# Performance work log

Hardware: AMD Instinct MI355X
Metric: run time of the kernel (lower is better)

Reference implementation:

```python
import jax, jax.numpy as jnp
import numpy as np

N_FEATURES = 256
HIDDEN = 16
BATCH = 32768


def setup_inputs() -> dict:
    key = jax.random.key(0)
    ks = jax.random.split(key, 8)
    F, H = N_FEATURES, HIDDEN
    x = jax.random.normal(ks[0], (BATCH, F), dtype=jnp.float32)
    # Stacked per-feature subnet params (torch Linear: y = x @ W.T + b)
    s1 = 1.0  # fan_in=1 for fc1
    W1 = jax.random.uniform(ks[1], (F, H), minval=-s1, maxval=s1, dtype=jnp.float32)
    b1 = jax.random.uniform(ks[2], (F, H), minval=-s1, maxval=s1, dtype=jnp.float32)
    s2 = 1.0 / np.sqrt(H)
    W2 = jax.random.uniform(ks[3], (F, H, H), minval=-s2, maxval=s2, dtype=jnp.float32)  # [F, out, in]
    b2 = jax.random.uniform(ks[4], (F, H), minval=-s2, maxval=s2, dtype=jnp.float32)
    W3 = jax.random.uniform(ks[5], (F, H), minval=-s2, maxval=s2, dtype=jnp.float32)  # out=1
    b3 = jax.random.uniform(ks[6], (F,), minval=-s2, maxval=s2, dtype=jnp.float32)
    linear_a = jnp.zeros((F,), dtype=jnp.float32)
    bias_b = jnp.zeros((1,), dtype=jnp.float32)
    return {"x": x, "linear_a": linear_a, "bias_b": bias_b,
            "W1": W1, "b1": b1, "W2": W2, "b2": b2, "W3": W3, "b3": b3}


def reference(x, linear_a, bias_b, W1, b1, W2, b2, W3, b3):
    # lin term: (x * a).sum(1)
    lin = x @ linear_a  # [B]
    # all subnets batched: h1 [B, F, H]
    h1 = jax.nn.relu(x[:, :, None] * W1[None, :, :] + b1[None, :, :])
    # fc2: y = h1 @ W2.T per feature; W2 is [F, out, in]
    h2 = jax.nn.relu(jnp.einsum('bfh,fkh->bfk', h1, W2) + b2[None, :, :])
    # fc3 -> scalar per feature, then sum over features
    out_f = jnp.einsum('bfh,fh->bf', h2, W3) + b3[None, :]  # [B, F]
    add_sum = out_f.sum(axis=1)  # [B]
    logits = lin + bias_b[0] + add_sum
    return logits
```

## Files before the change

### kernel.cpp

```cpp
#include <hip/hip_runtime.h>


typedef float    f32x4 __attribute__((ext_vector_type(4)));
typedef _Float16 f16x4 __attribute__((ext_vector_type(4)));
typedef __fp16   pk16x2 __attribute__((ext_vector_type(2)));

__device__ __forceinline__ f16x4 cvt4(f32x4 v) {
    pk16x2 lo = __builtin_amdgcn_cvt_pkrtz(v[0], v[1]);
    pk16x2 hi = __builtin_amdgcn_cvt_pkrtz(v[2], v[3]);
    union { unsigned u[2]; f16x4 h; } un;
    un.u[0] = __builtin_bit_cast(unsigned, lo);
    un.u[1] = __builtin_bit_cast(unsigned, hi);
    return un.h;
}

__device__ __forceinline__ f16x4 relu_h(f16x4 v) {
    f16x4 z = {};
    return __builtin_elementwise_max(v, z);
}

__device__ __forceinline__ f32x4 relu_f(f32x4 v) {
    f32x4 z = {0.f, 0.f, 0.f, 0.f};
    return __builtin_elementwise_max(v, z);
}

#define FCHUNK 16
#define BATCH  32768

__global__ __launch_bounds__(256, 8) void igann_kernel(
    const float* __restrict__ x,  const float* __restrict__ la,
    const float* __restrict__ bb, const float* __restrict__ W1,
    const float* __restrict__ b1, const float* __restrict__ W2,
    const float* __restrict__ b2, const float* __restrict__ W3,
    const float* __restrict__ b3, float* __restrict__ ws)
{
    const int tid = threadIdx.x;
    const int l   = tid & 63;
    const int w   = tid >> 6;
    const int r   = l & 15;
    const int g   = l >> 4;
    const int g4  = g * 4;

    const int bid = blockIdx.x;
    const int rb  = (bid & 7) + (((bid >> 3) & 15) << 3);
    const int fg  = bid >> 7;
    const int f0  = fg * FCHUNK;
    const int rowbase = rb * 256;

    __shared__ _Float16 xs [256 * 16];
    __shared__ _Float16 w2s[FCHUNK * 16 * 16];
    __shared__ float    wbs_sums[256];
    __shared__ float2   bws[FCHUNK * 16];
    _Float16* wbs = (_Float16*)wbs_sums;
    float*    sums = wbs_sums;

    {
        const int rr  = tid >> 2;
        const int c4g = tid & 3;
        const int sw  = (rr >> 2) & 3;
        #pragma unroll
        for (int it = 0; it < 4; ++it) {
            const int row = it * 64 + rr;
            f32x4 v = *(const f32x4*)(x + (size_t)(rowbase + row) * 256 + f0 + c4g * 4);
            *(f16x4*)(xs + row * 16 + ((c4g ^ sw) & 3) * 4) = cvt4(v);
        }
    }
    {
        const int f = tid >> 4, n = tid & 15;
        const int sw = (n >> 2) & 3;
        const float* src = W2 + ((size_t)(f0 + f) * 16 + n) * 16;
        _Float16* dst = w2s + (f * 16 + n) * 16;
        #pragma unroll
        for (int q = 0; q < 4; ++q) {
            f32x4 v = *(const f32x4*)(src + q * 4);
            *(f16x4*)(dst + ((q ^ sw) & 3) * 4) = cvt4(v);
        }
    }
    {
        const int f = tid >> 4, k = tid & 15;
        const int base = f * 32 + (k >> 2) * 8 + (k & 3);
        wbs[base]     = (_Float16)W1[(size_t)(f0 + f) * 16 + k];
        wbs[base + 4] = (_Float16)b1[(size_t)(f0 + f) * 16 + k];
    }
    {
        const int f = tid >> 4, n = tid & 15;
        bws[tid] = make_float2(b2[(size_t)(f0 + f) * 16 + n],
                               W3[(size_t)(f0 + f) * 16 + n]);
    }
    __syncthreads();

    const _Float16* xw  = xs + (w * 64 + r) * 16;
    const int       xsw = ((w * 64 + r) >> 2) & 3;
    const _Float16* w2p = w2s + r * 16 + ((g ^ ((r >> 2) & 3)) & 3) * 4;

    f32x4 acc[4];
    #pragma unroll
    for (int t = 0; t < 4; ++t) acc[t] = (f32x4){0.f, 0.f, 0.f, 0.f};

    for (int fi = 0; fi < FCHUNK; fi += 4) {
        const int xoff = (((fi >> 2) ^ xsw) & 3) * 4;
        f16x4 xv[4];
        #pragma unroll
        for (int t = 0; t < 4; ++t)
            xv[t] = *(const f16x4*)(xw + t * 256 + xoff);

        #pragma unroll
        for (int u = 0; u < 4; ++u) {
            const int f = fi + u;
            f16x4 w1h   = *(const f16x4*)(wbs + f * 32 + g * 8);
            f16x4 b1h   = *(const f16x4*)(wbs + f * 32 + g * 8 + 4);
            f16x4 bfrag = *(const f16x4*)(w2p + f * 256);
            const float2 bw = bws[f * 16 + r];
            const f32x4 cinit = {bw.x, bw.x, bw.x, bw.x};
            const f32x4 w3k4  = {bw.y, bw.y, bw.y, bw.y};

            #pragma unroll
            for (int t = 0; t < 4; ++t) {
                const _Float16 s = xv[t][u];
                f16x4 xb = {s, s, s, s};
                f16x4 h = relu_h(xb * w1h + b1h);
                f32x4 d = __builtin_amdgcn_mfma_f32_16x16x16f16(h, bfrag, cinit, 0, 0, 0);
                acc[t] = __builtin_elementwise_fma(relu_f(d), w3k4, acc[t]);
            }
        }
    }

    __syncthreads();

    #pragma unroll
    for (int t = 0; t < 4; ++t)
        #pragma unroll
        for (int j = 0; j < 4; ++j) {
            float v = acc[t][j];
            v += __shfl_xor(v, 1, 64);
            v += __shfl_xor(v, 2, 64);
            v += __shfl_xor(v, 4, 64);
            v += __shfl_xor(v, 8, 64);
            if (r == 0)
                sums[w * 64 + t * 16 + g4 + j] = v;
        }
    __syncthreads();

    float b3s = 0.f;
    #pragma unroll
    for (int c = 0; c < FCHUNK; ++c) b3s += b3[f0 + c];
    float lin = 0.f;
    {
        const int swe = (tid >> 2) & 3;
        #pragma unroll
        for (int gq = 0; gq < 4; ++gq) {
            f16x4 xv4 = *(const f16x4*)(xs + tid * 16 + ((gq ^ swe) & 3) * 4);
            #pragma unroll
            for (int e = 0; e < 4; ++e)
                lin = fmaf((float)xv4[e], la[f0 + gq * 4 + e], lin);
        }
    }
    ws[(size_t)fg * BATCH + rowbase + tid] = sums[tid] + lin + b3s;
}

__global__ __launch_bounds__(128) void igann_reduce(
    const float* __restrict__ ws, const float* __restrict__ bb,
    float* __restrict__ out)
{
    const int i = blockIdx.x * 128 + threadIdx.x;
    float s = bb[0];
    #pragma unroll
    for (int gq = 0; gq < 16; ++gq)
        s += ws[(size_t)gq * BATCH + i];
    out[i] = s;
}

extern "C" void kernel_launch(void* const* d_in, const int* in_sizes, int n_in,
                              void* d_out, int out_size, void* d_ws, size_t ws_size,
                              hipStream_t stream) {
    const float* x  = (const float*)d_in[0];
    const float* la = (const float*)d_in[1];
    const float* bb = (const float*)d_in[2];
    const float* W1 = (const float*)d_in[3];
    const float* b1 = (const float*)d_in[4];
    const float* W2 = (const float*)d_in[5];
    const float* b2 = (const float*)d_in[6];
    const float* W3 = (const float*)d_in[7];
    const float* b3 = (const float*)d_in[8];
    float* out = (float*)d_out;
    float* ws  = (float*)d_ws;

    dim3 grid(2048), block(256);
    hipLaunchKernelGGL(igann_kernel, grid, block, 0, stream,
                       x, la, bb, W1, b1, W2, b2, W3, b3, ws);
    hipLaunchKernelGGL(igann_reduce, dim3(256), dim3(128), 0, stream,
                       ws, bb, out);
}
```

Before: 105.8 us.

## Load x directly into registers with software prefetch, drop shared-memory x staging

Drops the shared-memory staging buffer for x. Each thread now loads its own x rows from global memory into registers, converting to fp16 one 4-feature group at a time while prefetching the next group. The linear term is accumulated in registers during the main loop and passed through a small shared array. This removes LDS writes and reads and the swizzle logic, but each lane's global loads are 16-byte strided accesses, 1 KB apart per row, which may coalesce worse and leave latency exposed. Four lanes per row also load the same x data redundantly.

```diff
diff --git a/kernel.cpp b/kernel.cpp
--- a/kernel.cpp
+++ b/kernel.cpp
@@ -47,24 +47,19 @@
     const int f0  = fg * FCHUNK;
     const int rowbase = rb * 256;
 
-    __shared__ _Float16 xs [256 * 16];
     __shared__ _Float16 w2s[FCHUNK * 16 * 16];
     __shared__ float    wbs_sums[256];
     __shared__ float2   bws[FCHUNK * 16];
-    _Float16* wbs = (_Float16*)wbs_sums;
+    __shared__ float    lins[256];
+    _Float16* wbs  = (_Float16*)wbs_sums;
     float*    sums = wbs_sums;
 
-    {
-        const int rr  = tid >> 2;
-        const int c4g = tid & 3;
-        const int sw  = (rr >> 2) & 3;
-        #pragma unroll
-        for (int it = 0; it < 4; ++it) {
-            const int row = it * 64 + rr;
-            f32x4 v = *(const f32x4*)(x + (size_t)(rowbase + row) * 256 + f0 + c4g * 4);
-            *(f16x4*)(xs + row * 16 + ((c4g ^ sw) & 3) * 4) = cvt4(v);
-        }
-    }
+    const float* xp0 = x + (size_t)(rowbase + w * 64 + r) * 256 + f0;
+    f32x4 xr[4];
+    #pragma unroll
+    for (int t = 0; t < 4; ++t)
+        xr[t] = *(const f32x4*)(xp0 + t * 4096);
+
     {
         const int f = tid >> 4, n = tid & 15;
         const int sw = (n >> 2) & 3;
@@ -89,24 +84,32 @@
     }
     __syncthreads();
 
-    const _Float16* xw  = xs + (w * 64 + r) * 16;
-    const int       xsw = ((w * 64 + r) >> 2) & 3;
     const _Float16* w2p = w2s + r * 16 + ((g ^ ((r >> 2) & 3)) & 3) * 4;
 
     f32x4 acc[4];
     #pragma unroll
     for (int t = 0; t < 4; ++t) acc[t] = (f32x4){0.f, 0.f, 0.f, 0.f};
+    float lin4[4] = {0.f, 0.f, 0.f, 0.f};
 
-    for (int fi = 0; fi < FCHUNK; fi += 4) {
-        const int xoff = (((fi >> 2) ^ xsw) & 3) * 4;
-        f16x4 xv[4];
+    #pragma unroll
+    for (int q = 0; q < 4; ++q) {
+        f16x4 xh[4];
+        #pragma unroll
+        for (int t = 0; t < 4; ++t) xh[t] = cvt4(xr[t]);
+        if (q < 3) {
+            #pragma unroll
+            for (int t = 0; t < 4; ++t)
+                xr[t] = *(const f32x4*)(xp0 + t * 4096 + (q + 1) * 4);
+        }
         #pragma unroll
         for (int t = 0; t < 4; ++t)
-            xv[t] = *(const f16x4*)(xw + t * 256 + xoff);
+            #pragma unroll
+            for (int u = 0; u < 4; ++u)
+                lin4[t] = fmaf((float)xh[t][u], la[f0 + q * 4 + u], lin4[t]);
 
         #pragma unroll
         for (int u = 0; u < 4; ++u) {
-            const int f = fi + u;
+            const int f = q * 4 + u;
             f16x4 w1h   = *(const f16x4*)(wbs + f * 32 + g * 8);
             f16x4 b1h   = *(const f16x4*)(wbs + f * 32 + g * 8 + 4);
             f16x4 bfrag = *(const f16x4*)(w2p + f * 256);
@@ -116,7 +119,7 @@
 
             #pragma unroll
             for (int t = 0; t < 4; ++t) {
-                const _Float16 s = xv[t][u];
+                const _Float16 s = xh[t][u];
                 f16x4 xb = {s, s, s, s};
                 f16x4 h = relu_h(xb * w1h + b1h);
                 f32x4 d = __builtin_amdgcn_mfma_f32_16x16x16f16(h, bfrag, cinit, 0, 0, 0);
@@ -127,6 +130,11 @@
 
     __syncthreads();
 
+    if (g == 0) {
+        #pragma unroll
+        for (int t = 0; t < 4; ++t)
+            lins[w * 64 + t * 16 + r] = lin4[t];
+    }
     #pragma unroll
     for (int t = 0; t < 4; ++t)
         #pragma unroll
@@ -144,18 +152,7 @@
     float b3s = 0.f;
     #pragma unroll
     for (int c = 0; c < FCHUNK; ++c) b3s += b3[f0 + c];
-    float lin = 0.f;
-    {
-        const int swe = (tid >> 2) & 3;
-        #pragma unroll
-        for (int gq = 0; gq < 4; ++gq) {
-            f16x4 xv4 = *(const f16x4*)(xs + tid * 16 + ((gq ^ swe) & 3) * 4);
-            #pragma unroll
-            for (int e = 0; e < 4; ++e)
-                lin = fmaf((float)xv4[e], la[f0 + gq * 4 + e], lin);
-        }
-    }
-    ws[(size_t)fg * BATCH + rowbase + tid] = sums[tid] + lin + b3s;
+    ws[(size_t)fg * BATCH + rowbase + tid] = sums[tid] + lins[tid] + b3s;
 }
 
 __global__ __launch_bounds__(128) void igann_reduce(
```

Result: slower. 224.1 us (+111.9%).

## Process two row tiles per block with prefetch of second x tile

Applied to the files above, without the earlier changes.

Each block now handles 512 rows instead of 256, so the W2/W1/bias staging is amortized over twice as many rows and the grid is halved. The second half's x tile is loaded into registers before computing the first half and written to a second shared buffer afterwards, overlapping global latency with MFMA work. Launch bounds drop to 4 blocks per SM to allow more registers, which may reduce occupancy and latency hiding. The block-to-row mapping also loses the previous interleaved rb swizzle.

```diff
diff --git a/kernel.cpp b/kernel.cpp
--- a/kernel.cpp
+++ b/kernel.cpp
@@ -27,7 +27,7 @@
 #define FCHUNK 16
 #define BATCH  32768
 
-__global__ __launch_bounds__(256, 8) void igann_kernel(
+__global__ __launch_bounds__(256, 4) void igann_kernel(
     const float* __restrict__ x,  const float* __restrict__ la,
     const float* __restrict__ bb, const float* __restrict__ W1,
     const float* __restrict__ b1, const float* __restrict__ W2,
@@ -42,38 +42,36 @@
     const int g4  = g * 4;
 
     const int bid = blockIdx.x;
-    const int rb  = (bid & 7) + (((bid >> 3) & 15) << 3);
-    const int fg  = bid >> 7;
+    const int rbb = bid & 63;
+    const int fg  = bid >> 6;
     const int f0  = fg * FCHUNK;
-    const int rowbase = rb * 256;
-
-    __shared__ _Float16 xs [256 * 16];
+    const int rowbase = rbb * 512;
+
+    __shared__ _Float16 xs [2][256 * 16];
     __shared__ _Float16 w2s[FCHUNK * 16 * 16];
-    __shared__ float    wbs_sums[256];
+    __shared__ _Float16 wbs[FCHUNK * 4 * 8];
     __shared__ float2   bws[FCHUNK * 16];
-    _Float16* wbs = (_Float16*)wbs_sums;
-    float*    sums = wbs_sums;
-
-    {
-        const int rr  = tid >> 2;
-        const int c4g = tid & 3;
-        const int sw  = (rr >> 2) & 3;
-        #pragma unroll
-        for (int it = 0; it < 4; ++it) {
-            const int row = it * 64 + rr;
-            f32x4 v = *(const f32x4*)(x + (size_t)(rowbase + row) * 256 + f0 + c4g * 4);
-            *(f16x4*)(xs + row * 16 + ((c4g ^ sw) & 3) * 4) = cvt4(v);
-        }
-    }
+    __shared__ float    sums[512];
+
+    const int rr  = tid >> 2;
+    const int c4g = tid & 3;
+    const int sw  = (rr >> 2) & 3;
+    const float* xsrc = x + (size_t)rowbase * 256 + f0 + c4g * 4;
+
+    f32x4 xa[4];
+    #pragma unroll
+    for (int it = 0; it < 4; ++it)
+        xa[it] = *(const f32x4*)(xsrc + (size_t)(it * 64 + rr) * 256);
+
     {
         const int f = tid >> 4, n = tid & 15;
-        const int sw = (n >> 2) & 3;
+        const int swn = (n >> 2) & 3;
         const float* src = W2 + ((size_t)(f0 + f) * 16 + n) * 16;
         _Float16* dst = w2s + (f * 16 + n) * 16;
         #pragma unroll
         for (int q = 0; q < 4; ++q) {
             f32x4 v = *(const f32x4*)(src + q * 4);
-            *(f16x4*)(dst + ((q ^ sw) & 3) * 4) = cvt4(v);
+            *(f16x4*)(dst + ((q ^ swn) & 3) * 4) = cvt4(v);
         }
     }
     {
@@ -87,75 +85,97 @@
         bws[tid] = make_float2(b2[(size_t)(f0 + f) * 16 + n],
                                W3[(size_t)(f0 + f) * 16 + n]);
     }
+    #pragma unroll
+    for (int it = 0; it < 4; ++it)
+        *(f16x4*)(xs[0] + (it * 64 + rr) * 16 + ((c4g ^ sw) & 3) * 4) = cvt4(xa[it]);
     __syncthreads();
 
-    const _Float16* xw  = xs + (w * 64 + r) * 16;
-    const int       xsw = ((w * 64 + r) >> 2) & 3;
+    f32x4 xb4[4];
+    #pragma unroll
+    for (int it = 0; it < 4; ++it)
+        xb4[it] = *(const f32x4*)(xsrc + (size_t)(256 + it * 64 + rr) * 256);
+
+    const int       rw  = w * 64 + r;
+    const int       xsw = (rw >> 2) & 3;
     const _Float16* w2p = w2s + r * 16 + ((g ^ ((r >> 2) & 3)) & 3) * 4;
 
-    f32x4 acc[4];
-    #pragma unroll
-    for (int t = 0; t < 4; ++t) acc[t] = (f32x4){0.f, 0.f, 0.f, 0.f};
-
-    for (int fi = 0; fi < FCHUNK; fi += 4) {
-        const int xoff = (((fi >> 2) ^ xsw) & 3) * 4;
-        f16x4 xv[4];
-        #pragma unroll
-        for (int t = 0; t < 4; ++t)
-            xv[t] = *(const f16x4*)(xw + t * 256 + xoff);
-
-        #pragma unroll
-        for (int u = 0; u < 4; ++u) {
-            const int f = fi + u;
-            f16x4 w1h   = *(const f16x4*)(wbs + f * 32 + g * 8);
-            f16x4 b1h   = *(const f16x4*)(wbs + f * 32 + g * 8 + 4);
-            f16x4 bfrag = *(const f16x4*)(w2p + f * 256);
-            const float2 bw = bws[f * 16 + r];
-            const f32x4 cinit = {bw.x, bw.x, bw.x, bw.x};
-            const f32x4 w3k4  = {bw.y, bw.y, bw.y, bw.y};
-
+    auto compute_half = [&](const _Float16* xsb, float* sh) {
+        const _Float16* xw = xsb + rw * 16;
+        f32x4 acc[4];
+        #pragma unroll
+        for (int t = 0; t < 4; ++t) acc[t] = (f32x4){0.f, 0.f, 0.f, 0.f};
+
+        for (int fi = 0; fi < FCHUNK; fi += 4) {
+            const int xoff = (((fi >> 2) ^ xsw) & 3) * 4;
+            f16x4 xv[4];
             #pragma unroll
-            for (int t = 0; t < 4; ++t) {
-                const _Float16 s = xv[t][u];
-                f16x4 xb = {s, s, s, s};
-                f16x4 h = relu_h(xb * w1h + b1h);
-                f32x4 d = __builtin_amdgcn_mfma_f32_16x16x16f16(h, bfrag, cinit, 0, 0, 0);
-                acc[t] = __builtin_elementwise_fma(relu_f(d), w3k4, acc[t]);
+            for (int t = 0; t < 4; ++t)
+                xv[t] = *(const f16x4*)(xw + t * 256 + xoff);
+
+            #pragma unroll
+            for (int u = 0; u < 4; ++u) {
+                const int f = fi + u;
+                f16x4 w1h   = *(const f16x4*)(wbs + f * 32 + g * 8);
+                f16x4 b1h   = *(const f16x4*)(wbs + f * 32 + g * 8 + 4);
+                f16x4 bfrag = *(const f16x4*)(w2p + f * 256);
+                const float2 bw = bws[f * 16 + r];
+                const f32x4 cinit = {bw.x, bw.x, bw.x, bw.x};
+                const f32x4 w3k4  = {bw.y, bw.y, bw.y, bw.y};
+
+                #pragma unroll
+                for (int t = 0; t < 4; ++t) {
+                    const _Float16 s = xv[t][u];
+                    f16x4 xb = {s, s, s, s};
+                    f16x4 h = relu_h(xb * w1h + b1h);
+                    f32x4 d = __builtin_amdgcn_mfma_f32_16x16x16f16(h, bfrag, cinit, 0, 0, 0);
+                    acc[t] = __builtin_elementwise_fma(relu_f(d), w3k4, acc[t]);
+                }
             }
         }
-    }
-
+        #pragma unroll
+        for (int t = 0; t < 4; ++t)
+            #pragma unroll
+            for (int j = 0; j < 4; ++j) {
+                float v = acc[t][j];
+                v += __shfl_xor(v, 1, 64);
+                v += __shfl_xor(v, 2, 64);
+                v += __shfl_xor(v, 4, 64);
+                v += __shfl_xor(v, 8, 64);
+                if (r == 0)
+                    sh[w * 64 + t * 16 + g4 + j] = v;
+            }
+    };
+
+    compute_half(xs[0], sums);
+
+    #pragma unroll
+    for (int it = 0; it < 4; ++it)
+        *(f16x4*)(xs[1] + (it * 64 + rr) * 16 + ((c4g ^ sw) & 3) * 4) = cvt4(xb4[it]);
     __syncthreads();
 
-    #pragma unroll
-    for (int t = 0; t < 4; ++t)
-        #pragma unroll
-        for (int j = 0; j < 4; ++j) {
-            float v = acc[t][j];
-            v += __shfl_xor(v, 1, 64);
-            v += __shfl_xor(v, 2, 64);
-            v += __shfl_xor(v, 4, 64);
-            v += __shfl_xor(v, 8, 64);
-            if (r == 0)
-                sums[w * 64 + t * 16 + g4 + j] = v;
+    compute_half(xs[1], sums + 256);
+    __syncthreads();
+
+    float b3s = 0.f;
+    #pragma unroll
+    for (int c = 0; c < FCHUNK; ++c) b3s += b3[f0 + c];
+    const int swe = (tid >> 2) & 3;
+    float lin0 = 0.f, lin1 = 0.f;
+    #pragma unroll
+    for (int gq = 0; gq < 4; ++gq) {
+        const int off = tid * 16 + ((gq ^ swe) & 3) * 4;
+        f16x4 a0 = *(const f16x4*)(xs[0] + off);
+        f16x4 a1 = *(const f16x4*)(xs[1] + off);
+        #pragma unroll
+        for (int e = 0; e < 4; ++e) {
+            const float lae = la[f0 + gq * 4 + e];
+            lin0 = fmaf((float)a0[e], lae, lin0);
+            lin1 = fmaf((float)a1[e], lae, lin1);
         }
-    __syncthreads();
-
-    float b3s = 0.f;
-    #pragma unroll
-    for (int c = 0; c < FCHUNK; ++c) b3s += b3[f0 + c];
-    float lin = 0.f;
-    {
-        const int swe = (tid >> 2) & 3;
-        #pragma unroll
-        for (int gq = 0; gq < 4; ++gq) {
-            f16x4 xv4 = *(const f16x4*)(xs + tid * 16 + ((gq ^ swe) & 3) * 4);
-            #pragma unroll
-            for (int e = 0; e < 4; ++e)
-                lin = fmaf((float)xv4[e], la[f0 + gq * 4 + e], lin);
-        }
-    }
-    ws[(size_t)fg * BATCH + rowbase + tid] = sums[tid] + lin + b3s;
+    }
+    float* wsp = ws + (size_t)fg * BATCH + rowbase;
+    wsp[tid]       = sums[tid]       + lin0 + b3s;
+    wsp[256 + tid] = sums[256 + tid] + lin1 + b3s;
 }
 
 __global__ __launch_bounds__(128) void igann_reduce(
@@ -185,7 +205,7 @@
     float* out = (float*)d_out;
     float* ws  = (float*)d_ws;
 
-    dim3 grid(2048), block(256);
+    dim3 grid(1024), block(256);
     hipLaunchKernelGGL(igann_kernel, grid, block, 0, stream,
                        x, la, bb, W1, b1, W2, b2, W3, b3, ws);
     hipLaunchKernelGGL(igann_reduce, dim3(256), dim3(128), 0, stream,
```

New measurement: 109.8 us. 3.8% more time.
